# Performance work log

Measured on AMD Instinct MI355X. Metric: run time of the kernel, lower is better.

The kernel has to match this reference:

```python
import jax, jax.numpy as jnp
import numpy as np
from jax import lax

B = 128
ROUTING_ITER = 3
EPS = 1e-9


def _conv(x, w, b, stride):
    y = lax.conv_general_dilated(x, w, window_strides=(stride, stride), padding='VALID',
                                 dimension_numbers=('NCHW', 'OIHW', 'NCHW'))
    return y + b[None, :, None, None]


def _squash(s):
    # squash along capsule dim (axis=3), s: [B,1,10,16,1]
    sq = jnp.sum(s * s, axis=3, keepdims=True)
    return (sq / (1.0 + sq)) * s / jnp.sqrt(sq + EPS)


def setup_inputs() -> dict:
    key = jax.random.key(0)
    ks = jax.random.split(key, 16)
    x = jax.random.normal(ks[0], (B, 1, 28, 28), dtype=jnp.float32)
    labels = jax.random.randint(ks[1], (B,), 0, 10)
    y = jax.nn.one_hot(labels, 10, dtype=jnp.float32)
    conv1_w = jax.random.normal(ks[2], (256, 1, 9, 9), dtype=jnp.float32) * 0.05
    conv1_b = jnp.zeros((256,), dtype=jnp.float32)
    caps1_w = jax.random.normal(ks[3], (256, 256, 9, 9), dtype=jnp.float32) * 0.01
    caps1_b = jnp.zeros((256,), dtype=jnp.float32)
    W = jax.random.normal(ks[4], (1, 1152, 10, 8, 16), dtype=jnp.float32) * 0.05
    caps_bias = jnp.zeros((1, 1, 10, 16, 1), dtype=jnp.float32)
    fc1_w = jax.random.normal(ks[5], (512, 16), dtype=jnp.float32) * 0.1
    fc1_b = jnp.zeros((512,), dtype=jnp.float32)
    fc2_w = jax.random.normal(ks[6], (1024, 512), dtype=jnp.float32) * 0.04
    fc2_b = jnp.zeros((1024,), dtype=jnp.float32)
    fc3_w = jax.random.normal(ks[7], (784, 1024), dtype=jnp.float32) * 0.03
    fc3_b = jnp.zeros((784,), dtype=jnp.float32)
    return {'x': x, 'y': y, 'conv1_w': conv1_w, 'conv1_b': conv1_b,
            'caps1_w': caps1_w, 'caps1_b': caps1_b, 'W': W, 'caps_bias': caps_bias,
            'fc1_w': fc1_w, 'fc1_b': fc1_b, 'fc2_w': fc2_w, 'fc2_b': fc2_b,
            'fc3_w': fc3_w, 'fc3_b': fc3_b}


def _forward(x, y, conv1_w, conv1_b, caps1_w, caps1_b, W, caps_bias,
             fc1_w, fc1_b, fc2_w, fc2_b, fc3_w, fc3_b):
    h = jax.nn.relu(_conv(x, conv1_w, conv1_b, 1))          # [B,256,20,20]
    h = jax.nn.relu(_conv(h, caps1_w, caps1_b, 2))          # [B,256,6,6]

    # faithful repeat+view layout from the torch code (NOT a transpose)
    x_view = jnp.tile(h.reshape(B, 256, 1, 6, 6), (1, 1, 10, 1, 1)).reshape(B, 1152, 10, 8, 1)
    W_view = jnp.broadcast_to(W, (B, 1152, 10, 8, 16)).reshape(B, 1152, 10, 16, 8)
    u_hat = jnp.matmul(W_view, x_view)                      # [B,1152,10,16,1]
    u_hat_stopped = lax.stop_gradient(u_hat)

    b_ij = jnp.zeros((B, 1152, 10, 1, 1), dtype=u_hat.dtype)
    V_J = None
    for r in range(ROUTING_ITER):
        c_ij = jax.nn.softmax(b_ij, axis=2)                 # softmax over 10 classes
        if r < ROUTING_ITER - 1:
            s_j = jnp.sum(c_ij * u_hat_stopped, axis=1, keepdims=True) + caps_bias
            v_j = _squash(s_j)                              # [B,1,10,16,1]
            # agreement: u_hat^T . v, [B,1152,10,1,16] @ [B,1152,10,16,1]
            agree = jnp.matmul(u_hat_stopped.reshape(B, 1152, 10, 1, 16),
                               jnp.broadcast_to(v_j, (B, 1152, 10, 16, 1)))
            b_ij = b_ij + agree
        else:
            s_j = jnp.sum(c_ij * u_hat, axis=1, keepdims=True) + caps_bias
            V_J = _squash(s_j)                              # [B,1,10,16,1]

    caps_out = jnp.squeeze(V_J, axis=1)                     # [B,10,16,1]
    v_length = jnp.sqrt(jnp.sum(caps_out * caps_out, axis=2, keepdims=True) + EPS)
    v_length = v_length.reshape(B, 10, 1, 1)

    # torch: squeeze -> [B,10,16], then .view(B,16,10) (reshape, not transpose)
    flat = caps_out.reshape(B, 10, 16).reshape(B, 16, 10)
    masked_v = jnp.matmul(flat, y.reshape(B, 10, 1)).reshape(B, 16)

    fc1 = masked_v @ fc1_w.T + fc1_b                        # no activation (faithful)
    fc2 = fc1 @ fc2_w.T + fc2_b
    reconstruction = jax.nn.sigmoid(fc2 @ fc3_w.T + fc3_b)  # [B,784]
    return v_length, reconstruction


def reference(x, y, conv1_w, conv1_b, caps1_w, caps1_b, W, caps_bias,
              fc1_w, fc1_b, fc2_w, fc2_b, fc3_w, fc3_b):
    return _forward(x, y, conv1_w, conv1_b, caps1_w, caps1_b, W, caps_bias,
                    fc1_w, fc1_b, fc2_w, fc2_b, fc3_w, fc3_b)
```

## Files before the change

### kernel.cpp

```cpp
#include <hip/hip_runtime.h>
#include <hip/hip_bf16.h>

typedef unsigned short ushort_t;
typedef __attribute__((ext_vector_type(8))) short short8;
typedef __attribute__((ext_vector_type(4))) float f32x4;


#define OFFB_H1T  0u
#define OFFB_WT   26214400u
#define OFFB_PART 36831232u
#define OFFB_H2   55705600u
#define OFFB_UH   60424192u
#define OFFB_BIJ  107610112u
#define OFFB_C    113508352u
#define OFFB_V    119406592u
#define OFFB_F1   119488512u
#define OFFB_F2   119750656u

__device__ __forceinline__ ushort_t f2bf(float f) {
  union { float f; unsigned int u; } c; c.f = f;
  unsigned int r = (c.u + 0x7FFFu + ((c.u >> 16) & 1u)) >> 16;
  return (ushort_t)r;
}
__device__ __forceinline__ float bf2f(ushort_t u) {
  union { unsigned int i; float f; } c; c.i = ((unsigned int)u) << 16;
  return c.f;
}

__global__ __launch_bounds__(256) void conv1_kernel(
    const float* __restrict__ x, const float* __restrict__ w,
    const float* __restrict__ bias, ushort_t* __restrict__ h1t) {
  int blk = blockIdx.x;
  int b = blk / 20, oy = blk % 20;
  int co = threadIdx.x;
  __shared__ float xs[252];
  for (int l = co; l < 252; l += 256)
    xs[l] = x[b * 784 + (oy + l / 28) * 28 + (l % 28)];
  __syncthreads();
  float bs = bias[co];
  float acc[20];
#pragma unroll
  for (int i = 0; i < 20; ++i) acc[i] = bs;
  for (int ky = 0; ky < 9; ++ky) {
    float xr[28];
#pragma unroll
    for (int i = 0; i < 28; ++i) xr[i] = xs[ky * 28 + i];
    float wk[9];
#pragma unroll
    for (int kx = 0; kx < 9; ++kx) wk[kx] = w[co * 81 + ky * 9 + kx];
#pragma unroll
    for (int kx = 0; kx < 9; ++kx)
#pragma unroll
      for (int ox = 0; ox < 20; ++ox) acc[ox] += wk[kx] * xr[ox + kx];
  }
  int xb = (b * 20 + oy) * 20;
#pragma unroll
  for (int ox = 0; ox < 20; ++ox)
    h1t[(xb + ox) * 256 + co] = f2bf(fmaxf(acc[ox], 0.f));
}

__global__ __launch_bounds__(256) void wreorder_kernel(
    const float* __restrict__ w, ushort_t* __restrict__ wt) {
  int co = blockIdx.x;
  __shared__ ushort_t wl[256 * 82];
  int t = threadIdx.x;
  const float* src = w + (size_t)co * 20736;
  for (int e = t; e < 20736; e += 256) {
    int ci = e / 81, kk = e - ci * 81;
    wl[ci * 82 + kk] = f2bf(src[e]);
  }
  __syncthreads();
  for (int kk = 0; kk < 81; ++kk)
    wt[((size_t)kk * 256 + co) * 256 + t] = wl[t * 82 + kk];
}

__global__ __launch_bounds__(256) void caps1_gemm(
    const ushort_t* __restrict__ h1t, const ushort_t* __restrict__ wt,
    float* __restrict__ part) {
  int lb = (blockIdx.x & 7) * 144 + (blockIdx.x >> 3);
  int chunk = lb / 288;
  int tile = lb - chunk * 288;
  int gm0 = (tile >> 2) * 64;
  int gn0 = (tile & 3) * 64;
  int ci0 = chunk << 6;
  int t = threadIdx.x;
  int wave = t >> 6, lane = t & 63;
  int wm = (wave >> 1) * 32, wn = (wave & 1) * 32;
  int lr = lane & 15, lg = lane >> 4;

  __shared__ __align__(16) ushort_t As[2][64 * 64];
  __shared__ __align__(16) ushort_t Bs[2][64 * 64];

  int r = t >> 2, seg = t & 3;
  int m = gm0 + r;
  int b = m / 36, pos = m - b * 36;
  int oy = pos / 6, ox = pos - oy * 6;
  const ushort_t* arow = h1t + ((b * 20 + 2 * oy) * 20 + 2 * ox) * 256 + ci0 + seg * 16;
  const ushort_t* brow = wt + (gn0 + r) * 256 + ci0 + seg * 16;
  int rx = r & 7;
  int st0 = r * 64 + (((seg << 1) | 0) ^ rx) * 8;
  int st1 = r * 64 + (((seg << 1) | 1) ^ rx) * 8;
  int lx = lr & 7;
  int sl0 = ((0 * 4 + lg) ^ lx) * 8;
  int sl1 = ((1 * 4 + lg) ^ lx) * 8;

  f32x4 acc[2][2];
#pragma unroll
  for (int i = 0; i < 2; ++i)
#pragma unroll
    for (int j = 0; j < 2; ++j)
#pragma unroll
      for (int e = 0; e < 4; ++e) acc[i][j][e] = 0.f;

  float4 ra0, ra1, rb0, rb1;
  ra0 = *(const float4*)(arow);
  ra1 = *(const float4*)(arow + 8);
  rb0 = *(const float4*)(brow);
  rb1 = *(const float4*)(brow + 8);
  *(float4*)&As[0][st0] = ra0;
  *(float4*)&As[0][st1] = ra1;
  *(float4*)&Bs[0][st0] = rb0;
  *(float4*)&Bs[0][st1] = rb1;
  __syncthreads();

  int buf = 0;
  for (int kk = 0; kk < 81; ++kk) {
    int nxt = kk + 1;
    if (nxt < 81) {
      int ky = nxt / 9, kx = nxt - ky * 9;
      const ushort_t* ap = arow + (ky * 20 + kx) * 256;
      ra0 = *(const float4*)(ap);
      ra1 = *(const float4*)(ap + 8);
      const ushort_t* bp = brow + nxt * 65536;
      rb0 = *(const float4*)(bp);
      rb1 = *(const float4*)(bp + 8);
    }
    short8 af[2][2], bfr[2][2];
#pragma unroll
    for (int mf = 0; mf < 2; ++mf) {
      int ra = (wm + mf * 16 + lr) * 64;
      af[mf][0] = *(const short8*)&As[buf][ra + sl0];
      af[mf][1] = *(const short8*)&As[buf][ra + sl1];
    }
#pragma unroll
    for (int nf = 0; nf < 2; ++nf) {
      int rb = (wn + nf * 16 + lr) * 64;
      bfr[nf][0] = *(const short8*)&Bs[buf][rb + sl0];
      bfr[nf][1] = *(const short8*)&Bs[buf][rb + sl1];
    }
#pragma unroll
    for (int kh = 0; kh < 2; ++kh)
#pragma unroll
      for (int mf = 0; mf < 2; ++mf)
#pragma unroll
        for (int nf = 0; nf < 2; ++nf)
          acc[mf][nf] = __builtin_amdgcn_mfma_f32_16x16x32_bf16(
              af[mf][kh], bfr[nf][kh], acc[mf][nf], 0, 0, 0);
    __syncthreads();
    if (nxt < 81) {
      int nb = buf ^ 1;
      *(float4*)&As[nb][st0] = ra0;
      *(float4*)&As[nb][st1] = ra1;
      *(float4*)&Bs[nb][st0] = rb0;
      *(float4*)&Bs[nb][st1] = rb1;
      __syncthreads();
    }
    buf ^= 1;
  }

#pragma unroll
  for (int mf = 0; mf < 2; ++mf)
#pragma unroll
    for (int nf = 0; nf < 2; ++nf) {
      int nn = gn0 + wn + nf * 16 + lr;
#pragma unroll
      for (int reg = 0; reg < 4; ++reg) {
        int mm = gm0 + wm + mf * 16 + lg * 4 + reg;
        part[((size_t)chunk * 4608 + mm) * 256 + nn] = acc[mf][nf][reg];
      }
    }
}

__global__ __launch_bounds__(256) void reduce_kernel(
    const float* __restrict__ part, const float* __restrict__ bias,
    float* __restrict__ h2) {
  int m = blockIdx.x;
  int n = threadIdx.x;
  size_t o = (size_t)m * 256 + n;
  float s = part[o] + part[o + 4608 * 256] + part[o + 2 * 4608 * 256] +
            part[o + 3 * 4608 * 256];
  h2[o] = fmaxf(s + bias[n], 0.f);
}

__global__ __launch_bounds__(256) void uhat_kernel(
    const float* __restrict__ h2, const float* __restrict__ W,
    ushort_t* __restrict__ uh) {
  int blk = blockIdx.x;
  int bh = blk & 1;
  int qpc = blk >> 1;
  int q = qpc / 72;
  int pc = qpc - q * 72;
  int p0 = pc * 16;
  int b0 = bh * 64;
  __shared__ float Wl[16][132];
  __shared__ float xl[64][16][9];
  int t = threadIdx.x;
#pragma unroll
  for (int it = 0; it < 2; ++it) {
    int idx = t * 2 + it;
    int row = idx >> 5;
    int c4 = idx & 31;
    float4 vv = *(reinterpret_cast<const float4*>(
        &W[(size_t)((p0 + row) * 10 + q) * 128]) + c4);
    Wl[row][c4 * 4 + 0] = vv.x;
    Wl[row][c4 * 4 + 1] = vv.y;
    Wl[row][c4 * 4 + 2] = vv.z;
    Wl[row][c4 * 4 + 3] = vv.w;
  }
  for (int j = 0; j < 32; ++j) {
    int e = t + 256 * j;
    int b_l = e >> 7;
    int rem = e & 127;
    int i = rem >> 3, n = rem & 7;
    int f = (p0 + i) * 80 + q * 8 + n;
    xl[b_l][i][n] = h2[((size_t)(b0 + b_l) * 36 + (f % 36)) * 256 + (f / 360)];
  }
  __syncthreads();
  int p_l = t & 15;
  int b_ll = t >> 4;
  const float* wr = &Wl[p_l][0];
#pragma unroll
  for (int k = 0; k < 4; ++k) {
    int b_l = b_ll + 16 * k;
    float xv[8];
#pragma unroll
    for (int n = 0; n < 8; ++n) xv[n] = xl[b_l][p_l][n];
    short8 o0, o1;
#pragma unroll
    for (int a = 0; a < 8; ++a) {
      float ue = 0.f, uo = 0.f;
#pragma unroll
      for (int n = 0; n < 8; ++n) {
        ue += wr[a * 16 + n] * xv[n];
        uo += wr[a * 16 + 8 + n] * xv[n];
      }
      if (a < 4) { o0[2 * a] = (short)f2bf(ue); o0[2 * a + 1] = (short)f2bf(uo); }
      else { o1[2 * (a - 4)] = (short)f2bf(ue); o1[2 * (a - 4) + 1] = (short)f2bf(uo); }
    }
    size_t dst = ((size_t)((b0 + b_l) * 10 + q) * 1152 + p0 + p_l) * 16;
    *(short8*)&uh[dst] = o0;
    *(short8*)&uh[dst + 8] = o1;
  }
}

template <int MODE>
__global__ __launch_bounds__(64) void sv_kernel(
    const ushort_t* __restrict__ uh, const float* __restrict__ cbuf,
    const float* __restrict__ caps_bias, float* __restrict__ v,
    float* __restrict__ out) {
  int bq = blockIdx.x;
  int q = bq % 10;
  int t = threadIdx.x;
  const ushort_t* ub = &uh[(size_t)bq * 1152 * 16];
  const float* cb = &cbuf[(size_t)bq * 1152];
  float s[16];
#pragma unroll
  for (int m = 0; m < 16; ++m) s[m] = 0.f;
  for (int p = t; p < 1152; p += 64) {
    short8 u0 = *(const short8*)&ub[p * 16];
    short8 u1 = *(const short8*)&ub[p * 16 + 8];
    float c = (MODE == 0) ? 0.1f : cb[p];
#pragma unroll
    for (int m = 0; m < 8; ++m) s[m] += c * bf2f((ushort_t)u0[m]);
#pragma unroll
    for (int m = 0; m < 8; ++m) s[8 + m] += c * bf2f((ushort_t)u1[m]);
  }
#pragma unroll
  for (int m = 0; m < 16; ++m) {
    float val = s[m];
#pragma unroll
    for (int off = 32; off > 0; off >>= 1) val += __shfl_down(val, off);
    s[m] = val;
  }
  if (t == 0) {
    float sq = 0.f;
#pragma unroll
    for (int m = 0; m < 16; ++m) {
      s[m] += caps_bias[q * 16 + m];
      sq += s[m] * s[m];
    }
    float coef = (sq / (1.f + sq)) * rsqrtf(sq + 1e-9f);
    float vl2 = 0.f;
#pragma unroll
    for (int m = 0; m < 16; ++m) {
      float vv = coef * s[m];
      v[bq * 16 + m] = vv;
      vl2 += vv * vv;
    }
    if (MODE == 2) out[bq] = sqrtf(vl2 + 1e-9f);
  }
}

template <bool FIRST>
__global__ __launch_bounds__(256) void agree_kernel(
    const ushort_t* __restrict__ uh, const float* __restrict__ v,
    float* __restrict__ bij, float* __restrict__ cbuf) {
  int tid = blockIdx.x * 256 + threadIdx.x;
  int b = tid / 1152;
  int p = tid - b * 1152;
  float br[10];
  float* bp = &bij[(size_t)tid * 10];
#pragma unroll
  for (int q = 0; q < 10; ++q) {
    const ushort_t* ub = &uh[(size_t)((b * 10 + q) * 1152 + p) * 16];
    short8 u0 = *(const short8*)ub;
    short8 u1 = *(const short8*)(ub + 8);
    const float4* v4 = reinterpret_cast<const float4*>(&v[(b * 10 + q) * 16]);
    float4 b0 = v4[0], b1 = v4[1], b2 = v4[2], b3 = v4[3];
    float d = bf2f((ushort_t)u0[0]) * b0.x + bf2f((ushort_t)u0[1]) * b0.y
            + bf2f((ushort_t)u0[2]) * b0.z + bf2f((ushort_t)u0[3]) * b0.w
            + bf2f((ushort_t)u0[4]) * b1.x + bf2f((ushort_t)u0[5]) * b1.y
            + bf2f((ushort_t)u0[6]) * b1.z + bf2f((ushort_t)u0[7]) * b1.w
            + bf2f((ushort_t)u1[0]) * b2.x + bf2f((ushort_t)u1[1]) * b2.y
            + bf2f((ushort_t)u1[2]) * b2.z + bf2f((ushort_t)u1[3]) * b2.w
            + bf2f((ushort_t)u1[4]) * b3.x + bf2f((ushort_t)u1[5]) * b3.y
            + bf2f((ushort_t)u1[6]) * b3.z + bf2f((ushort_t)u1[7]) * b3.w;
    br[q] = (FIRST ? 0.f : bp[q]) + d;
  }
  float mx = br[0];
#pragma unroll
  for (int q = 1; q < 10; ++q) mx = fmaxf(mx, br[q]);
  float den = 0.f;
  float ex[10];
#pragma unroll
  for (int q = 0; q < 10; ++q) { ex[q] = __expf(br[q] - mx); den += ex[q]; }
  float inv = 1.f / den;
#pragma unroll
  for (int q = 0; q < 10; ++q) {
    bp[q] = br[q];
    cbuf[(size_t)(b * 10 + q) * 1152 + p] = ex[q] * inv;
  }
}

__global__ __launch_bounds__(128) void fc1_kernel(
    const float* __restrict__ v, const float* __restrict__ y,
    const float* __restrict__ fc1_w, const float* __restrict__ fc1_b,
    float* __restrict__ f1g) {
  int b = blockIdx.x, t = threadIdx.x;
  __shared__ float mv[16];
  if (t < 16) {
    const float* vb = &v[b * 160];
    float a = 0.f;
#pragma unroll
    for (int tt = 0; tt < 10; ++tt) a += vb[t * 10 + tt] * y[b * 10 + tt];
    mv[t] = a;
  }
  __syncthreads();
  for (int o = t; o < 512; o += 128) {
    const float4* wr = reinterpret_cast<const float4*>(&fc1_w[o * 16]);
    float4 w0 = wr[0], w1 = wr[1], w2 = wr[2], w3 = wr[3];
    f1g[b * 512 + o] = fc1_b[o]
        + mv[0] * w0.x + mv[1] * w0.y + mv[2] * w0.z + mv[3] * w0.w
        + mv[4] * w1.x + mv[5] * w1.y + mv[6] * w1.z + mv[7] * w1.w
        + mv[8] * w2.x + mv[9] * w2.y + mv[10] * w2.z + mv[11] * w2.w
        + mv[12] * w3.x + mv[13] * w3.y + mv[14] * w3.z + mv[15] * w3.w;
  }
}

__global__ __launch_bounds__(256) void fc2_kernel(
    const float* __restrict__ f1g, const float* __restrict__ fc2_w,
    const float* __restrict__ fc2_b, float* __restrict__ f2g) {
  int b = blockIdx.x >> 2;
  int o = (blockIdx.x & 3) * 256 + threadIdx.x;
  __shared__ float f1[512];
  for (int l = threadIdx.x; l < 512; l += 256) f1[l] = f1g[b * 512 + l];
  __syncthreads();
  const float4* wr = reinterpret_cast<const float4*>(&fc2_w[o * 512]);
  float a = fc2_b[o];
#pragma unroll 4
  for (int k4 = 0; k4 < 128; ++k4) {
    float4 w4 = wr[k4];
    a += f1[4 * k4] * w4.x + f1[4 * k4 + 1] * w4.y + f1[4 * k4 + 2] * w4.z +
         f1[4 * k4 + 3] * w4.w;
  }
  f2g[b * 1024 + o] = a;
}

__global__ __launch_bounds__(256) void fc3_kernel(
    const float* __restrict__ f2g, const float* __restrict__ fc3_w,
    const float* __restrict__ fc3_b, float* __restrict__ out) {
  int b = blockIdx.x >> 2;
  int oc = (blockIdx.x & 3) * 196;
  __shared__ float f2[1024];
  for (int l = threadIdx.x; l < 1024; l += 256) f2[l] = f2g[b * 1024 + l];
  __syncthreads();
  if (threadIdx.x >= 196) return;
  int o = oc + threadIdx.x;
  const float4* wr = reinterpret_cast<const float4*>(&fc3_w[o * 1024]);
  float a = fc3_b[o];
#pragma unroll 4
  for (int k4 = 0; k4 < 256; ++k4) {
    float4 w4 = wr[k4];
    a += f2[4 * k4] * w4.x + f2[4 * k4 + 1] * w4.y + f2[4 * k4 + 2] * w4.z +
         f2[4 * k4 + 3] * w4.w;
  }
  out[1280 + b * 784 + o] = 1.f / (1.f + __expf(-a));
}

extern "C" void kernel_launch(void* const* d_in, const int* in_sizes, int n_in,
                              void* d_out, int out_size, void* d_ws, size_t ws_size,
                              hipStream_t stream) {
  const float* x       = (const float*)d_in[0];
  const float* y       = (const float*)d_in[1];
  const float* conv1_w = (const float*)d_in[2];
  const float* conv1_b = (const float*)d_in[3];
  const float* caps1_w = (const float*)d_in[4];
  const float* caps1_b = (const float*)d_in[5];
  const float* W       = (const float*)d_in[6];
  const float* cbias   = (const float*)d_in[7];
  const float* fc1_w   = (const float*)d_in[8];
  const float* fc1_b   = (const float*)d_in[9];
  const float* fc2_w   = (const float*)d_in[10];
  const float* fc2_b   = (const float*)d_in[11];
  const float* fc3_w   = (const float*)d_in[12];
  const float* fc3_b   = (const float*)d_in[13];
  float* out = (float*)d_out;

  char* wsb = (char*)d_ws;
  ushort_t* h1t  = (ushort_t*)(wsb + OFFB_H1T);
  ushort_t* wt   = (ushort_t*)(wsb + OFFB_WT);
  float*    part = (float*)(wsb + OFFB_PART);
  float*    h2   = (float*)(wsb + OFFB_H2);
  ushort_t* uh   = (ushort_t*)(wsb + OFFB_UH);
  float*    bij  = (float*)(wsb + OFFB_BIJ);
  float*    c    = (float*)(wsb + OFFB_C);
  float*    v    = (float*)(wsb + OFFB_V);
  float*    f1   = (float*)(wsb + OFFB_F1);
  float*    f2   = (float*)(wsb + OFFB_F2);

  conv1_kernel<<<2560, 256, 0, stream>>>(x, conv1_w, conv1_b, h1t);
  wreorder_kernel<<<256, 256, 0, stream>>>(caps1_w, wt);
  caps1_gemm<<<1152, 256, 0, stream>>>(h1t, wt, part);
  reduce_kernel<<<4608, 256, 0, stream>>>(part, caps1_b, h2);
  uhat_kernel<<<1440, 256, 0, stream>>>(h2, W, uh);

  sv_kernel<0><<<1280, 64, 0, stream>>>(uh, c, cbias, v, out);
  agree_kernel<true><<<576, 256, 0, stream>>>(uh, v, bij, c);
  sv_kernel<1><<<1280, 64, 0, stream>>>(uh, c, cbias, v, out);
  agree_kernel<false><<<576, 256, 0, stream>>>(uh, v, bij, c);
  sv_kernel<2><<<1280, 64, 0, stream>>>(uh, c, cbias, v, out);

  fc1_kernel<<<128, 128, 0, stream>>>(v, y, fc1_w, fc1_b, f1);
  fc2_kernel<<<512, 256, 0, stream>>>(f1, fc2_w, fc2_b, f2);
  fc3_kernel<<<512, 256, 0, stream>>>(f2, fc3_w, fc3_b, out);
}
```

Before: 327.3 us.

## Rewrite caps1 GEMM as single-wave register-blocked MFMA without LDS; transpose conv1 weights

The caps1 GEMM drops the 4-wave LDS double-buffered scheme. Each block is now one wave that computes the whole 64x64 tile with a 4x4 grid of MFMA fragments, loading operands straight from global memory into registers with ping-pong prefetch. This removes the LDS stores and the barriers each k-step, at the cost of high register pressure, non-coalesced 16-byte global loads, and fewer waves to hide latency. Separately, conv1 weights are transposed by a small kernel so that per-thread weight loads become coalesced across output channels.

```diff
diff --git a/kernel.cpp b/kernel.cpp
--- a/kernel.cpp
+++ b/kernel.cpp
@@ -16,6 +16,7 @@
 #define OFFB_V    119406592u
 #define OFFB_F1   119488512u
 #define OFFB_F2   119750656u
+#define OFFB_W1T  120274944u
 
 __device__ __forceinline__ ushort_t f2bf(float f) {
   union { float f; unsigned int u; } c; c.f = f;
@@ -27,8 +28,15 @@
   return c.f;
 }
 
+__global__ __launch_bounds__(256) void w1t_kernel(
+    const float* __restrict__ w, float* __restrict__ w1t) {
+  int kk = blockIdx.x;
+  int co = threadIdx.x;
+  w1t[kk * 256 + co] = w[co * 81 + kk];
+}
+
 __global__ __launch_bounds__(256) void conv1_kernel(
-    const float* __restrict__ x, const float* __restrict__ w,
+    const float* __restrict__ x, const float* __restrict__ w1t,
     const float* __restrict__ bias, ushort_t* __restrict__ h1t) {
   int blk = blockIdx.x;
   int b = blk / 20, oy = blk % 20;
@@ -47,7 +55,7 @@
     for (int i = 0; i < 28; ++i) xr[i] = xs[ky * 28 + i];
     float wk[9];
 #pragma unroll
-    for (int kx = 0; kx < 9; ++kx) wk[kx] = w[co * 81 + ky * 9 + kx];
+    for (int kx = 0; kx < 9; ++kx) wk[kx] = w1t[(ky * 9 + kx) * 256 + co];
 #pragma unroll
     for (int kx = 0; kx < 9; ++kx)
 #pragma unroll
@@ -74,7 +82,7 @@
     wt[((size_t)kk * 256 + co) * 256 + t] = wl[t * 82 + kk];
 }
 
-__global__ __launch_bounds__(256) void caps1_gemm(
+__global__ __launch_bounds__(64) void caps1_gemm(
     const ushort_t* __restrict__ h1t, const ushort_t* __restrict__ wt,
     float* __restrict__ part) {
   int lb = (blockIdx.x & 7) * 144 + (blockIdx.x >> 3);
@@ -83,102 +91,81 @@
   int gm0 = (tile >> 2) * 64;
   int gn0 = (tile & 3) * 64;
   int ci0 = chunk << 6;
-  int t = threadIdx.x;
-  int wave = t >> 6, lane = t & 63;
-  int wm = (wave >> 1) * 32, wn = (wave & 1) * 32;
+  int lane = threadIdx.x;
   int lr = lane & 15, lg = lane >> 4;
 
-  __shared__ __align__(16) ushort_t As[2][64 * 64];
-  __shared__ __align__(16) ushort_t Bs[2][64 * 64];
-
-  int r = t >> 2, seg = t & 3;
-  int m = gm0 + r;
-  int b = m / 36, pos = m - b * 36;
-  int oy = pos / 6, ox = pos - oy * 6;
-  const ushort_t* arow = h1t + ((b * 20 + 2 * oy) * 20 + 2 * ox) * 256 + ci0 + seg * 16;
-  const ushort_t* brow = wt + (gn0 + r) * 256 + ci0 + seg * 16;
-  int rx = r & 7;
-  int st0 = r * 64 + (((seg << 1) | 0) ^ rx) * 8;
-  int st1 = r * 64 + (((seg << 1) | 1) ^ rx) * 8;
-  int lx = lr & 7;
-  int sl0 = ((0 * 4 + lg) ^ lx) * 8;
-  int sl1 = ((1 * 4 + lg) ^ lx) * 8;
-
-  f32x4 acc[2][2];
-#pragma unroll
-  for (int i = 0; i < 2; ++i)
-#pragma unroll
-    for (int j = 0; j < 2; ++j)
+  const ushort_t* ab[4];
+#pragma unroll
+  for (int mf = 0; mf < 4; ++mf) {
+    int m = gm0 + mf * 16 + lr;
+    int b = m / 36, pos = m - b * 36;
+    int oy = pos / 6, ox = pos - oy * 6;
+    ab[mf] = h1t + ((b * 20 + 2 * oy) * 20 + 2 * ox) * 256 + ci0 + lg * 8;
+  }
+  const ushort_t* bb[4];
+#pragma unroll
+  for (int nf = 0; nf < 4; ++nf)
+    bb[nf] = wt + (size_t)(gn0 + nf * 16 + lr) * 256 + ci0 + lg * 8;
+
+  f32x4 acc[4][4];
+#pragma unroll
+  for (int i = 0; i < 4; ++i)
+#pragma unroll
+    for (int j = 0; j < 4; ++j)
 #pragma unroll
       for (int e = 0; e < 4; ++e) acc[i][j][e] = 0.f;
 
-  float4 ra0, ra1, rb0, rb1;
-  ra0 = *(const float4*)(arow);
-  ra1 = *(const float4*)(arow + 8);
-  rb0 = *(const float4*)(brow);
-  rb1 = *(const float4*)(brow + 8);
-  *(float4*)&As[0][st0] = ra0;
-  *(float4*)&As[0][st1] = ra1;
-  *(float4*)&Bs[0][st0] = rb0;
-  *(float4*)&Bs[0][st1] = rb1;
-  __syncthreads();
-
-  int buf = 0;
-  for (int kk = 0; kk < 81; ++kk) {
-    int nxt = kk + 1;
-    if (nxt < 81) {
-      int ky = nxt / 9, kx = nxt - ky * 9;
-      const ushort_t* ap = arow + (ky * 20 + kx) * 256;
-      ra0 = *(const float4*)(ap);
-      ra1 = *(const float4*)(ap + 8);
-      const ushort_t* bp = brow + nxt * 65536;
-      rb0 = *(const float4*)(bp);
-      rb1 = *(const float4*)(bp + 8);
-    }
-    short8 af[2][2], bfr[2][2];
-#pragma unroll
-    for (int mf = 0; mf < 2; ++mf) {
-      int ra = (wm + mf * 16 + lr) * 64;
-      af[mf][0] = *(const short8*)&As[buf][ra + sl0];
-      af[mf][1] = *(const short8*)&As[buf][ra + sl1];
-    }
-#pragma unroll
-    for (int nf = 0; nf < 2; ++nf) {
-      int rb = (wn + nf * 16 + lr) * 64;
-      bfr[nf][0] = *(const short8*)&Bs[buf][rb + sl0];
-      bfr[nf][1] = *(const short8*)&Bs[buf][rb + sl1];
-    }
-#pragma unroll
-    for (int kh = 0; kh < 2; ++kh)
-#pragma unroll
-      for (int mf = 0; mf < 2; ++mf)
-#pragma unroll
-        for (int nf = 0; nf < 2; ++nf)
-          acc[mf][nf] = __builtin_amdgcn_mfma_f32_16x16x32_bf16(
-              af[mf][kh], bfr[nf][kh], acc[mf][nf], 0, 0, 0);
-    __syncthreads();
-    if (nxt < 81) {
-      int nb = buf ^ 1;
-      *(float4*)&As[nb][st0] = ra0;
-      *(float4*)&As[nb][st1] = ra1;
-      *(float4*)&Bs[nb][st0] = rb0;
-      *(float4*)&Bs[nb][st1] = rb1;
-      __syncthreads();
-    }
-    buf ^= 1;
-  }
-
-#pragma unroll
-  for (int mf = 0; mf < 2; ++mf)
-#pragma unroll
-    for (int nf = 0; nf < 2; ++nf) {
-      int nn = gn0 + wn + nf * 16 + lr;
+  short8 aA[4][2], bA[4][2], aB[4][2], bB[4][2];
+
+#define LDA(dst, kkv)                                                    \
+  {                                                                      \
+    int ky_ = (kkv) / 9, kx_ = (kkv) - ky_ * 9;                          \
+    int off_ = (ky_ * 20 + kx_) * 256;                                   \
+    _Pragma("unroll") for (int mf_ = 0; mf_ < 4; ++mf_)                  \
+        _Pragma("unroll") for (int kh_ = 0; kh_ < 2; ++kh_)              \
+            dst[mf_][kh_] = *(const short8*)(ab[mf_] + off_ + kh_ * 32); \
+  }
+#define LDB(dst, kkv)                                                    \
+  {                                                                      \
+    size_t off_ = (size_t)(kkv)*65536;                                   \
+    _Pragma("unroll") for (int nf_ = 0; nf_ < 4; ++nf_)                  \
+        _Pragma("unroll") for (int kh_ = 0; kh_ < 2; ++kh_)              \
+            dst[nf_][kh_] = *(const short8*)(bb[nf_] + off_ + kh_ * 32); \
+  }
+#define MM(af, bf)                                                       \
+  _Pragma("unroll") for (int kh_ = 0; kh_ < 2; ++kh_)                    \
+      _Pragma("unroll") for (int mf_ = 0; mf_ < 4; ++mf_)                \
+          _Pragma("unroll") for (int nf_ = 0; nf_ < 4; ++nf_)            \
+              acc[mf_][nf_] = __builtin_amdgcn_mfma_f32_16x16x32_bf16(   \
+                  af[mf_][kh_], bf[nf_][kh_], acc[mf_][nf_], 0, 0, 0);
+
+  LDA(aA, 0);
+  LDB(bA, 0);
+  for (int kk = 0; kk < 80; kk += 2) {
+    LDA(aB, kk + 1);
+    LDB(bB, kk + 1);
+    MM(aA, bA);
+    LDA(aA, kk + 2);
+    LDB(bA, kk + 2);
+    MM(aB, bB);
+  }
+  MM(aA, bA);
+
+  float* pbase = part + (size_t)chunk * 4608 * 256;
+#pragma unroll
+  for (int mf = 0; mf < 4; ++mf)
+#pragma unroll
+    for (int nf = 0; nf < 4; ++nf) {
+      int nn = gn0 + nf * 16 + lr;
 #pragma unroll
       for (int reg = 0; reg < 4; ++reg) {
-        int mm = gm0 + wm + mf * 16 + lg * 4 + reg;
-        part[((size_t)chunk * 4608 + mm) * 256 + nn] = acc[mf][nf][reg];
+        int mm = gm0 + mf * 16 + lg * 4 + reg;
+        pbase[(size_t)mm * 256 + nn] = acc[mf][nf][reg];
       }
     }
+#undef LDA
+#undef LDB
+#undef MM
 }
 
 __global__ __launch_bounds__(256) void reduce_kernel(
@@ -437,10 +424,12 @@
   float*    v    = (float*)(wsb + OFFB_V);
   float*    f1   = (float*)(wsb + OFFB_F1);
   float*    f2   = (float*)(wsb + OFFB_F2);
-
-  conv1_kernel<<<2560, 256, 0, stream>>>(x, conv1_w, conv1_b, h1t);
+  float*    w1t  = (float*)(wsb + OFFB_W1T);
+
+  w1t_kernel<<<81, 256, 0, stream>>>(conv1_w, w1t);
+  conv1_kernel<<<2560, 256, 0, stream>>>(x, w1t, conv1_b, h1t);
   wreorder_kernel<<<256, 256, 0, stream>>>(caps1_w, wt);
-  caps1_gemm<<<1152, 256, 0, stream>>>(h1t, wt, part);
+  caps1_gemm<<<1152, 64, 0, stream>>>(h1t, wt, part);
   reduce_kernel<<<4608, 256, 0, stream>>>(part, caps1_b, h2);
   uhat_kernel<<<1440, 256, 0, stream>>>(h2, W, uh);
 
```

Result: slower. 417.4 us (+27.5%).
